# Kernel tuning notes

Hardware: AMD Instinct MI355X
Metric: run time of the kernel (lower is better)

Reference implementation:

```python
import jax, jax.numpy as jnp
import numpy as np

B, S, D, H = 4, 2048, 1024, 16
HD = D // H  # head_dim = 64


def setup_inputs() -> dict:
    key = jax.random.key(0)
    k1, k2, k3, k4, k5 = jax.random.split(key, 5)
    x = jax.random.normal(k1, (B, S, D), dtype=jnp.float32)
    # per-head QKV projection weights (H separate Linear(D, 3*HD) layers, batched)
    Wqkv = jax.random.normal(k2, (H, D, 3 * HD), dtype=jnp.float32) * (D ** -0.5)
    bqkv = jax.random.normal(k3, (H, 3 * HD), dtype=jnp.float32) * 0.02
    # output projection Linear(D, D)
    Wo = jax.random.normal(k4, (D, D), dtype=jnp.float32) * (D ** -0.5)
    bo = jax.random.normal(k5, (D,), dtype=jnp.float32) * 0.02
    return {"x": x, "Wqkv": Wqkv, "bqkv": bqkv, "Wo": Wo, "bo": bo}


def reference(x, Wqkv, bqkv, Wo, bo):
    # Batched per-head QKV projection: [B,S,D] x [H,D,3*HD] -> [B,H,S,3*HD]
    qkv = jnp.einsum('bsd,hde->bhse', x, Wqkv) + bqkv[None, :, None, :]
    q, k, v = jnp.split(qkv, 3, axis=-1)  # each [B,H,S,HD]
    scale = HD ** -0.5
    scores = jnp.einsum('bhqe,bhke->bhqk', q, k) * scale  # [B,H,S,S]
    causal = jnp.tril(jnp.ones((S, S), dtype=bool))
    scores = jnp.where(causal, scores, -jnp.inf)
    attn = jax.nn.softmax(scores, axis=-1)
    # dropout is identity in eval mode
    out = jnp.einsum('bhqk,bhke->bhqe', attn, v)  # [B,H,S,HD]
    out = jnp.transpose(out, (0, 2, 1, 3)).reshape(B, S, D)  # concat heads
    return out @ Wo + bo
```

## Files before the change

kernel.cpp:

```cpp
#include <hip/hip_runtime.h>
#include <hip/hip_bf16.h>

#define B_ 4
#define S_ 2048
#define D_ 1024
#define H_ 16
#define HD_ 64
#define M_TOK 8192
#define QSCALE 0.18033688f

typedef __attribute__((ext_vector_type(4))) float f32x4;
typedef __attribute__((ext_vector_type(4))) int int4_t;
typedef __attribute__((ext_vector_type(8))) short short8;
typedef __attribute__((ext_vector_type(4))) short short4_t;

__device__ inline short f2bf(float f) {
  unsigned u = __builtin_bit_cast(unsigned, f);
  u += 0x7fff + ((u >> 16) & 1);
  return (short)(u >> 16);
}
__device__ inline short f2bf_trunc(float f) {
  return (short)(__builtin_bit_cast(unsigned, f) >> 16);
}
__device__ inline unsigned pack_bf16_trunc(float lo, float hi) {
  return __builtin_amdgcn_perm(__builtin_bit_cast(unsigned, hi),
                               __builtin_bit_cast(unsigned, lo), 0x07060302u);
}

typedef __attribute__((address_space(1))) const unsigned int gas_u32;
typedef __attribute__((address_space(3))) unsigned int las_u32;
__device__ inline void gload_lds16(const void* g, void* l) {
  __builtin_amdgcn_global_load_lds((gas_u32*)g, (las_u32*)l, 16, 0, 0);
}


__global__ __launch_bounds__(256) void conv_x_kernel(
    const float* __restrict__ x, short* __restrict__ xb) {
  size_t base = ((size_t)blockIdx.x * 256 + threadIdx.x) * 8;
  f32x4 v0 = *reinterpret_cast<const f32x4*>(&x[base]);
  f32x4 v1 = *reinterpret_cast<const f32x4*>(&x[base + 4]);
  short8 o;
  o[0]=f2bf(v0[0]); o[1]=f2bf(v0[1]); o[2]=f2bf(v0[2]); o[3]=f2bf(v0[3]);
  o[4]=f2bf(v1[0]); o[5]=f2bf(v1[1]); o[6]=f2bf(v1[2]); o[7]=f2bf(v1[3]);
  *reinterpret_cast<short8*>(&xb[base]) = o;
}

__global__ __launch_bounds__(256) void conv_wqkv_kernel(
    const float* __restrict__ Wqkv, short* __restrict__ wp) {
  const int h = blockIdx.x;
  const int k0 = blockIdx.y * 32;
  const int tid = threadIdx.x;
  __shared__ short T[192 * 40];
#pragma unroll
  for (int i = 0; i < 6; ++i) {
    int iv = tid + i * 256;
    int k = iv / 48;
    int e4 = (iv % 48) * 4;
    f32x4 v = *reinterpret_cast<const f32x4*>(&Wqkv[((size_t)h * D_ + k0 + k) * 192 + e4]);
#pragma unroll
    for (int j = 0; j < 4; ++j) T[(e4 + j) * 40 + k] = f2bf(v[j]);
  }
  __syncthreads();
#pragma unroll
  for (int i = 0; i < 3; ++i) {
    int u = tid + i * 256;
    int e16 = u >> 6;
    int rem = u & 63;
    int e = e16 * 16 + (rem & 15);
    int k8 = (rem >> 4) * 8;
    short8 o = *reinterpret_cast<const short8*>(&T[e * 40 + k8]);
    *reinterpret_cast<short8*>(
        &wp[(size_t)(h * 12 + e16) * 16384 + blockIdx.y * 512 + rem * 8]) = o;
  }
}

__global__ __launch_bounds__(256) void conv_wo_kernel(
    const float* __restrict__ Wo, short* __restrict__ wp) {
  const int k0 = blockIdx.x * 32;
  const int n0 = blockIdx.y * 128;
  const int tid = threadIdx.x;
  __shared__ short T[128 * 40];
#pragma unroll
  for (int i = 0; i < 4; ++i) {
    int iv = tid + i * 256;
    int k = iv >> 5;
    int n4 = (iv & 31) * 4;
    f32x4 v = *reinterpret_cast<const f32x4*>(&Wo[(size_t)(k0 + k) * 1024 + n0 + n4]);
#pragma unroll
    for (int j = 0; j < 4; ++j) T[(n4 + j) * 40 + k] = f2bf(v[j]);
  }
  __syncthreads();
#pragma unroll
  for (int i = 0; i < 2; ++i) {
    int u = tid + i * 256;
    int ntile = u >> 6;
    int rem = u & 63;
    short8 o = *reinterpret_cast<const short8*>(
        &T[(ntile * 16 + (rem & 15)) * 40 + (rem >> 4) * 8]);
    *reinterpret_cast<short8*>(
        &wp[(size_t)((n0 >> 4) + ntile) * 16384 + blockIdx.x * 512 + rem * 8]) = o;
  }
}

template<int EPI>
__global__ __launch_bounds__(256, 3) void gemm4_kernel(
    const short* __restrict__ A, const short* __restrict__ Bp,
    const float* __restrict__ bias,
    short* __restrict__ qb, short* __restrict__ kb, short* __restrict__ vt,
    float* __restrict__ out) {
  constexpr int KD = 1024;
  const int m0 = blockIdx.x * 128;
  const int n0 = blockIdx.y * 128;
  const int tid = threadIdx.x;
  const int lane = tid & 63, wv = tid >> 6;
  const int wr = wv >> 1, wc = wv & 1;
  const int g = lane >> 4, c = lane & 15;

  __shared__ short As[4 * 4096];

  const f32x4 zero4 = {0.f, 0.f, 0.f, 0.f};
  f32x4 acc[4][4];
#pragma unroll
  for (int i = 0; i < 4; ++i)
#pragma unroll
    for (int j = 0; j < 4; ++j) acc[i][j] = zero4;

  const short* bbase = Bp + (size_t)((n0 + wc * 64) >> 4) * 16384 + lane * 8;
  short8 bb0[4], bb1[4];

  auto LOADB = [&](int t, short8* br) {
#pragma unroll
    for (int nt = 0; nt < 4; ++nt)
      br[nt] = *reinterpret_cast<const short8*>(&bbase[(size_t)nt * 16384 + t * 512]);
  };
  auto STAGE = [&](int kt, int buf) {
    const short* asrc = A + (size_t)m0 * KD + kt * 32;
#pragma unroll
    for (int i = 0; i < 2; ++i) {
      int ch = tid + i * 256;
      int row = ch >> 2;
      int slot = (ch & 3) ^ ((row >> 1) & 3);
      gload_lds16(asrc + (size_t)row * KD + slot * 8, &As[buf * 4096 + ch * 8]);
    }
  };
  const int sread = (g ^ ((c >> 1) & 3)) * 8;
  auto COMP = [&](int buf, short8* br) {
    const short* Ab = &As[buf * 4096];
    short8 a[4];
#pragma unroll
    for (int mt = 0; mt < 4; ++mt)
      a[mt] = *reinterpret_cast<const short8*>(&Ab[(wr * 64 + mt * 16 + c) * 32 + sread]);
    __builtin_amdgcn_s_setprio(1);
#pragma unroll
    for (int mt = 0; mt < 4; ++mt)
#pragma unroll
      for (int nt = 0; nt < 4; ++nt)
        acc[mt][nt] = __builtin_amdgcn_mfma_f32_16x16x32_bf16(a[mt], br[nt], acc[mt][nt], 0, 0, 0);
    __builtin_amdgcn_s_setprio(0);
  };

#define BAR1 __builtin_amdgcn_sched_barrier(0); __builtin_amdgcn_s_barrier(); __builtin_amdgcn_sched_barrier(0)
#define VMW(N) asm volatile("s_waitcnt vmcnt(" #N ")" ::: "memory")

  STAGE(0, 0); STAGE(1, 1); LOADB(0, bb0);

#pragma unroll 1
  for (int p = 0; p < 7; ++p) {
    const int tb = p * 4;
    BAR1; STAGE(tb + 2, 2); LOADB(tb + 1, bb1); VMW(6); BAR1; COMP(0, bb0);
    BAR1; STAGE(tb + 3, 3); LOADB(tb + 2, bb0); VMW(6); BAR1; COMP(1, bb1);
    BAR1; STAGE(tb + 4, 0); LOADB(tb + 3, bb1); VMW(6); BAR1; COMP(2, bb0);
    BAR1; STAGE(tb + 5, 1); LOADB(tb + 4, bb0); VMW(6); BAR1; COMP(3, bb1);
  }
  BAR1; STAGE(30, 2); LOADB(29, bb1); VMW(6); BAR1; COMP(0, bb0);
  BAR1; STAGE(31, 3); LOADB(30, bb0); VMW(6); BAR1; COMP(1, bb1);
  BAR1;               LOADB(31, bb1); VMW(4); BAR1; COMP(2, bb0);
  BAR1;                               VMW(0); BAR1; COMP(3, bb1);

#undef BAR1
#undef VMW

  if (EPI == 0) {
#pragma unroll
    for (int nt = 0; nt < 4; ++nt) {
      int n = n0 + wc * 64 + nt * 16 + c;
      float bv = bias[n];
      int h = n / 192, e = n % 192;
      if (e < 128) {
#pragma unroll
        for (int mt = 0; mt < 4; ++mt) {
          int m_base = m0 + wr * 64 + mt * 16 + g * 4;
          int bb2 = m_base >> 11, s0 = m_base & 2047;
          size_t plane = (size_t)(bb2 * H_ + h) * (S_ * HD_);
          if (e < 64) {
            size_t bp = plane + (size_t)(s0 >> 4) * 1024 + (e >> 3) * 128 + (s0 & 15) * 8 + (e & 7);
#pragma unroll
            for (int r = 0; r < 4; ++r)
              qb[bp + r * 8] = f2bf((acc[mt][nt][r] + bv) * QSCALE);
          } else {
            int ek = e - 64;
            size_t bp = plane + (size_t)(s0 >> 4) * 1024 + (ek >> 3) * 128 + (s0 & 15) * 8 + (ek & 7);
#pragma unroll
            for (int r = 0; r < 4; ++r)
              kb[bp + r * 8] = f2bf(acc[mt][nt][r] + bv);
          }
        }
      } else {
        int hd = e - 128;
#pragma unroll
        for (int mtp = 0; mtp < 2; ++mtp) {
          int mt = mtp * 2;
          int m_base = m0 + wr * 64 + mt * 16 + g * 4;
          int bb2 = m_base >> 11, s0 = m_base & 2047;
          size_t plane = (size_t)(bb2 * H_ + h) * (S_ * HD_);
          size_t bp = plane + (size_t)((hd >> 4) * 64 + (s0 >> 5)) * 512 +
                      ((s0 >> 2) & 3) * 128 + (hd & 15) * 8;
          int4_t pk;
#pragma unroll
          for (int r = 0; r < 4; ++r)
            pk[r] = (int)pack_bf16_trunc(acc[mt][nt][r] + bv, acc[mt + 1][nt][r] + bv);
          *reinterpret_cast<int4_t*>(&vt[bp]) = pk;
        }
      }
    }
  } else {
#pragma unroll
    for (int mt = 0; mt < 4; ++mt) {
#pragma unroll
      for (int nt = 0; nt < 4; ++nt) {
        int n = n0 + wc * 64 + nt * 16 + c;
        float bv = bias[n];
        int m_base = m0 + wr * 64 + mt * 16 + g * 4;
#pragma unroll
        for (int r = 0; r < 4; ++r)
          out[(size_t)(m_base + r) * D_ + n] = acc[mt][nt][r] + bv;
      }
    }
  }
}

struct KF32 { short8 f[4]; };

__device__ __forceinline__ void load_kf32(KF32& k, const short* __restrict__ kbh,
                                          int ktb, int lane) {
#pragma unroll
  for (int cc = 0; cc < 2; ++cc)
#pragma unroll
    for (int t = 0; t < 2; ++t)
      k.f[cc * 2 + t] = *reinterpret_cast<const short8*>(
          &kbh[(size_t)(ktb * 2 + t) * 1024 + cc * 512 + lane * 8]);
}

__global__ __launch_bounds__(256, 3) void attn_kernel(
    const short* __restrict__ qb, const short* __restrict__ kb,
    const short* __restrict__ vt, short* __restrict__ av) {
  const int orig = blockIdx.x;
  const int xcd = orig & 7;
  const int local = orig >> 3;
  const int bh = xcd * 8 + (local & 7);
  const int qt = 15 - (local >> 3);
  const int bb = bh >> 4, h = bh & 15;
  const int tid = threadIdx.x;
  const int lane = tid & 63, wv = tid >> 6;
  const int g = lane >> 4, c = lane & 15;
  const int q0 = qt * 128;
  const int r0 = q0 + wv * 32;

  __shared__ short Ps[4][32 * 40];
  short* Pw = Ps[wv];
  unsigned* Pw32 = reinterpret_cast<unsigned*>(Pw);

  const short* qbh = qb + (size_t)bh * S_ * HD_;
  const short* kbh = kb + (size_t)bh * S_ * HD_;
  const short* vth = vt + (size_t)bh * HD_ * S_;

  short8 ones;
#pragma unroll
  for (int j = 0; j < 8; ++j) ones[j] = (short)0x3F80;

  const f32x4 zero4 = {0.f, 0.f, 0.f, 0.f};

  short8 qf[2][2];
#pragma unroll
  for (int mt = 0; mt < 2; ++mt)
#pragma unroll
    for (int cc = 0; cc < 2; ++cc)
      qf[mt][cc] = *reinterpret_cast<const short8*>(
          &qbh[(size_t)(r0 / 16 + mt) * 1024 + cc * 512 + lane * 8]);

  f32x4 acc_o[2][4];
  f32x4 lacc[2];
#pragma unroll
  for (int mt = 0; mt < 2; ++mt) {
    lacc[mt] = zero4;
#pragma unroll
    for (int nt = 0; nt < 4; ++nt) acc_o[mt][nt] = zero4;
  }

  const int diag = 4 * qt + wv;
  const int nk = diag + 1;

  KF32 kA, kB;
  load_kf32(kA, kbh, 0, lane);

  auto body = [&](int ktb, KF32& kc, KF32& kn) {
    const int k0 = ktb * 32;
    short8 vf[4];
#pragma unroll
    for (int nt = 0; nt < 4; ++nt)
      vf[nt] = *reinterpret_cast<const short8*>(
          &vth[(size_t)(nt * 64 + ktb) * 512 + lane * 8]);
    f32x4 sc[2][2];
#pragma unroll
    for (int mt = 0; mt < 2; ++mt)
#pragma unroll
      for (int t = 0; t < 2; ++t) sc[mt][t] = zero4;
#pragma unroll
    for (int cc = 0; cc < 2; ++cc)
#pragma unroll
      for (int mt = 0; mt < 2; ++mt)
#pragma unroll
        for (int t = 0; t < 2; ++t)
          sc[mt][t] = __builtin_amdgcn_mfma_f32_16x16x32_bf16(
              qf[mt][cc], kc.f[cc * 2 + t], sc[mt][t], 0, 0, 0);
    int ktbn = ktb + 1;
    if (ktbn >= S_ / 32) ktbn = 0;
    load_kf32(kn, kbh, ktbn, lane);
    if (ktb == diag) {
#pragma unroll
      for (int mt = 0; mt < 2; ++mt)
#pragma unroll
        for (int t = 0; t < 2; ++t) {
          const int key = k0 + t * 16 + c;
#pragma unroll
          for (int r = 0; r < 4; ++r) {
            const int qi2 = r0 + mt * 16 + g * 4 + r;
            if (key > qi2) sc[mt][t][r] = -INFINITY;
          }
        }
    }
#pragma unroll
    for (int mt = 0; mt < 2; ++mt)
#pragma unroll
      for (int r = 0; r < 4; ++r) {
        float p0 = __builtin_exp2f(sc[mt][0][r]);
        float p1 = __builtin_exp2f(sc[mt][1][r]);
        Pw32[(mt * 16 + g * 4 + r) * 20 + c] = pack_bf16_trunc(p0, p1);
      }
    short8 pa[2];
#pragma unroll
    for (int mt = 0; mt < 2; ++mt)
      pa[mt] = *reinterpret_cast<const short8*>(&Pw[(mt * 16 + c) * 40 + g * 8]);
#pragma unroll
    for (int mt = 0; mt < 2; ++mt)
      lacc[mt] = __builtin_amdgcn_mfma_f32_16x16x32_bf16(pa[mt], ones, lacc[mt], 0, 0, 0);
#pragma unroll
    for (int mt = 0; mt < 2; ++mt)
#pragma unroll
      for (int nt = 0; nt < 4; ++nt)
        acc_o[mt][nt] = __builtin_amdgcn_mfma_f32_16x16x32_bf16(
            pa[mt], vf[nt], acc_o[mt][nt], 0, 0, 0);
  };

  int ktb = 0;
  for (; ktb + 1 < nk; ktb += 2) {
    body(ktb,     kA, kB);
    body(ktb + 1, kB, kA);
  }
  if (ktb < nk) body(ktb, kA, kB);

#pragma unroll
  for (int mt = 0; mt < 2; ++mt) {
    float inv[4];
#pragma unroll
    for (int r = 0; r < 4; ++r) inv[r] = 1.0f / lacc[mt][r];
#pragma unroll
    for (int nt = 0; nt < 4; ++nt)
#pragma unroll
      for (int r = 0; r < 4; ++r) {
        int R = r0 + mt * 16 + g * 4 + r;
        av[(size_t)(bb * S_ + R) * D_ + h * HD_ + nt * 16 + c] =
            f2bf(acc_o[mt][nt][r] * inv[r]);
      }
  }
}

extern "C" void kernel_launch(void* const* d_in, const int* in_sizes, int n_in,
                              void* d_out, int out_size, void* d_ws, size_t ws_size,
                              hipStream_t stream) {
  const float* x    = (const float*)d_in[0];
  const float* Wqkv = (const float*)d_in[1];
  const float* bqkv = (const float*)d_in[2];
  const float* Wo   = (const float*)d_in[3];
  const float* bo   = (const float*)d_in[4];
  float* out = (float*)d_out;

  const size_t NTOK = (size_t)B_ * H_ * S_ * HD_;
  short* xb    = (short*)d_ws;
  short* wqkvt = xb + (size_t)M_TOK * D_;
  short* wot   = wqkvt + (size_t)3072 * 1024;
  short* qb    = wot + (size_t)1024 * 1024;
  short* kb    = qb + NTOK;
  short* vt    = kb + NTOK;
  short* av    = xb;

  conv_x_kernel   <<<4096, 256, 0, stream>>>(x, xb);
  conv_wqkv_kernel<<<dim3(16, 32), 256, 0, stream>>>(Wqkv, wqkvt);
  conv_wo_kernel  <<<dim3(32, 8), 256, 0, stream>>>(Wo, wot);
  gemm4_kernel<0> <<<dim3(64, 24), 256, 0, stream>>>(xb, wqkvt, bqkv, qb, kb, vt, nullptr);
  attn_kernel     <<<1024, 256, 0, stream>>>(qb, kb, vt, av);
  gemm4_kernel<1> <<<dim3(64, 8), 256, 0, stream>>>(av, wot, bo, nullptr, nullptr, nullptr, out);
}
```

Measured before the change: 160.5 us.

## Restructure GEMM mainloop to 64-wide K stages with triple-buffered LDS

Rewrites the bf16 GEMM main loop so each A stage covers 64 K elements (8-chunk XOR swizzle) in a 3-slot LDS ring instead of 32-wide stages in 4 slots. Each barrier pair now covers two K-halves of MFMA work, and B fragments are prefetched two tiles ahead with four register sets. The aim is to halve barrier and waitcnt overhead per unit of compute. In exchange it uses more LDS (48KB vs 32KB) and more registers, which may cut occupancy at 3 blocks per CU.

```diff
diff --git a/kernel.cpp b/kernel.cpp
--- a/kernel.cpp
+++ b/kernel.cpp
@@ -103,7 +103,7 @@
 }
 
 template<int EPI>
-__global__ __launch_bounds__(256, 3) void gemm4_kernel(
+__global__ __launch_bounds__(256, 3) void gemm5_kernel(
     const short* __restrict__ A, const short* __restrict__ Bp,
     const float* __restrict__ bias,
     short* __restrict__ qb, short* __restrict__ kb, short* __restrict__ vt,
@@ -116,7 +116,7 @@
   const int wr = wv >> 1, wc = wv & 1;
   const int g = lane >> 4, c = lane & 15;
 
-  __shared__ short As[4 * 4096];
+  __shared__ short As[3 * 8192];
 
   const f32x4 zero4 = {0.f, 0.f, 0.f, 0.f};
   f32x4 acc[4][4];
@@ -126,30 +126,31 @@
     for (int j = 0; j < 4; ++j) acc[i][j] = zero4;
 
   const short* bbase = Bp + (size_t)((n0 + wc * 64) >> 4) * 16384 + lane * 8;
-  short8 bb0[4], bb1[4];
+  short8 bb0[4], bb1[4], bb2[4], bb3[4];
 
   auto LOADB = [&](int t, short8* br) {
 #pragma unroll
     for (int nt = 0; nt < 4; ++nt)
       br[nt] = *reinterpret_cast<const short8*>(&bbase[(size_t)nt * 16384 + t * 512]);
   };
-  auto STAGE = [&](int kt, int buf) {
-    const short* asrc = A + (size_t)m0 * KD + kt * 32;
-#pragma unroll
-    for (int i = 0; i < 2; ++i) {
+  auto STAGE64 = [&](int kt64, int buf) {
+    const short* asrc = A + (size_t)m0 * KD + kt64 * 64;
+#pragma unroll
+    for (int i = 0; i < 4; ++i) {
       int ch = tid + i * 256;
-      int row = ch >> 2;
-      int slot = (ch & 3) ^ ((row >> 1) & 3);
-      gload_lds16(asrc + (size_t)row * KD + slot * 8, &As[buf * 4096 + ch * 8]);
+      int row = ch >> 3;
+      int sub = ch & 7;
+      int slot = sub ^ (row & 7);
+      gload_lds16(asrc + (size_t)row * KD + slot * 8, &As[buf * 8192 + ch * 8]);
     }
   };
-  const int sread = (g ^ ((c >> 1) & 3)) * 8;
-  auto COMP = [&](int buf, short8* br) {
-    const short* Ab = &As[buf * 4096];
+  auto COMP = [&](int buf, int kh, short8* br) {
+    const short* Ab = &As[buf * 8192];
+    const int chx = ((g + kh * 4) ^ (c & 7)) * 8;
     short8 a[4];
 #pragma unroll
     for (int mt = 0; mt < 4; ++mt)
-      a[mt] = *reinterpret_cast<const short8*>(&Ab[(wr * 64 + mt * 16 + c) * 32 + sread]);
+      a[mt] = *reinterpret_cast<const short8*>(&Ab[(wr * 64 + mt * 16 + c) * 64 + chx]);
     __builtin_amdgcn_s_setprio(1);
 #pragma unroll
     for (int mt = 0; mt < 4; ++mt)
@@ -162,20 +163,29 @@
 #define BAR1 __builtin_amdgcn_sched_barrier(0); __builtin_amdgcn_s_barrier(); __builtin_amdgcn_sched_barrier(0)
 #define VMW(N) asm volatile("s_waitcnt vmcnt(" #N ")" ::: "memory")
 
-  STAGE(0, 0); STAGE(1, 1); LOADB(0, bb0);
-
+  STAGE64(0, 0); STAGE64(1, 1); LOADB(0, bb0); LOADB(1, bb1);
+
+  int e = 0;
 #pragma unroll 1
   for (int p = 0; p < 7; ++p) {
-    const int tb = p * 4;
-    BAR1; STAGE(tb + 2, 2); LOADB(tb + 1, bb1); VMW(6); BAR1; COMP(0, bb0);
-    BAR1; STAGE(tb + 3, 3); LOADB(tb + 2, bb0); VMW(6); BAR1; COMP(1, bb1);
-    BAR1; STAGE(tb + 4, 0); LOADB(tb + 3, bb1); VMW(6); BAR1; COMP(2, bb0);
-    BAR1; STAGE(tb + 5, 1); LOADB(tb + 4, bb0); VMW(6); BAR1; COMP(3, bb1);
-  }
-  BAR1; STAGE(30, 2); LOADB(29, bb1); VMW(6); BAR1; COMP(0, bb0);
-  BAR1; STAGE(31, 3); LOADB(30, bb0); VMW(6); BAR1; COMP(1, bb1);
-  BAR1;               LOADB(31, bb1); VMW(4); BAR1; COMP(2, bb0);
-  BAR1;                               VMW(0); BAR1; COMP(3, bb1);
+    const int o = (e + 1 == 3) ? 0 : e + 1;
+    const int s = (o + 1 == 3) ? 0 : o + 1;
+    BAR1; STAGE64(2 * p + 2, s); LOADB(4 * p + 2, bb2); LOADB(4 * p + 3, bb3);
+    VMW(12); BAR1;
+    COMP(e, 0, bb0); COMP(e, 1, bb1);
+    BAR1; STAGE64(2 * p + 3, e); LOADB(4 * p + 4, bb0); LOADB(4 * p + 5, bb1);
+    VMW(12); BAR1;
+    COMP(o, 0, bb2); COMP(o, 1, bb3);
+    e = s;
+  }
+  {
+    const int o = (e + 1 == 3) ? 0 : e + 1;
+    BAR1; LOADB(30, bb2); LOADB(31, bb3);
+    VMW(8); BAR1;
+    COMP(e, 0, bb0); COMP(e, 1, bb1);
+    VMW(0);
+    COMP(o, 0, bb2); COMP(o, 1, bb3);
+  }
 
 #undef BAR1
 #undef VMW
@@ -185,20 +195,20 @@
     for (int nt = 0; nt < 4; ++nt) {
       int n = n0 + wc * 64 + nt * 16 + c;
       float bv = bias[n];
-      int h = n / 192, e = n % 192;
-      if (e < 128) {
+      int h = n / 192, ee = n % 192;
+      if (ee < 128) {
 #pragma unroll
         for (int mt = 0; mt < 4; ++mt) {
           int m_base = m0 + wr * 64 + mt * 16 + g * 4;
-          int bb2 = m_base >> 11, s0 = m_base & 2047;
-          size_t plane = (size_t)(bb2 * H_ + h) * (S_ * HD_);
-          if (e < 64) {
-            size_t bp = plane + (size_t)(s0 >> 4) * 1024 + (e >> 3) * 128 + (s0 & 15) * 8 + (e & 7);
+          int bb2i = m_base >> 11, s0 = m_base & 2047;
+          size_t plane = (size_t)(bb2i * H_ + h) * (S_ * HD_);
+          if (ee < 64) {
+            size_t bp = plane + (size_t)(s0 >> 4) * 1024 + (ee >> 3) * 128 + (s0 & 15) * 8 + (ee & 7);
 #pragma unroll
             for (int r = 0; r < 4; ++r)
               qb[bp + r * 8] = f2bf((acc[mt][nt][r] + bv) * QSCALE);
           } else {
-            int ek = e - 64;
+            int ek = ee - 64;
             size_t bp = plane + (size_t)(s0 >> 4) * 1024 + (ek >> 3) * 128 + (s0 & 15) * 8 + (ek & 7);
 #pragma unroll
             for (int r = 0; r < 4; ++r)
@@ -206,13 +216,13 @@
           }
         }
       } else {
-        int hd = e - 128;
+        int hd = ee - 128;
 #pragma unroll
         for (int mtp = 0; mtp < 2; ++mtp) {
           int mt = mtp * 2;
           int m_base = m0 + wr * 64 + mt * 16 + g * 4;
-          int bb2 = m_base >> 11, s0 = m_base & 2047;
-          size_t plane = (size_t)(bb2 * H_ + h) * (S_ * HD_);
+          int bb2i = m_base >> 11, s0 = m_base & 2047;
+          size_t plane = (size_t)(bb2i * H_ + h) * (S_ * HD_);
           size_t bp = plane + (size_t)((hd >> 4) * 64 + (s0 >> 5)) * 512 +
                       ((s0 >> 2) & 3) * 128 + (hd & 15) * 8;
           int4_t pk;
@@ -407,7 +417,7 @@
   conv_x_kernel   <<<4096, 256, 0, stream>>>(x, xb);
   conv_wqkv_kernel<<<dim3(16, 32), 256, 0, stream>>>(Wqkv, wqkvt);
   conv_wo_kernel  <<<dim3(32, 8), 256, 0, stream>>>(Wo, wot);
-  gemm4_kernel<0> <<<dim3(64, 24), 256, 0, stream>>>(xb, wqkvt, bqkv, qb, kb, vt, nullptr);
+  gemm5_kernel<0> <<<dim3(64, 24), 256, 0, stream>>>(xb, wqkvt, bqkv, qb, kb, vt, nullptr);
   attn_kernel     <<<1024, 256, 0, stream>>>(qb, kb, vt, av);
-  gemm4_kernel<1> <<<dim3(64, 8), 256, 0, stream>>>(av, wot, bo, nullptr, nullptr, nullptr, out);
-}
+  gemm5_kernel<1> <<<dim3(64, 8), 256, 0, stream>>>(av, wot, bo, nullptr, nullptr, nullptr, out);
+}
```

After: 177.5 us. +10.6%, slower.

## Replace QKV projection GEMM with 256x128-tile 512-thread kernel and XCD-aware mapping

Applied to the files above, without the earlier changes.

The QKV projection GEMM moves to a new kernel using 512-thread blocks with 256x128 output tiles and K-steps of 64 held in swizzled LDS. A triple-buffered register set for B fragments is fully unrolled, and a 1D grid remaps block ids so each XCD handles a fixed group of N columns. The aim is more reuse per loaded A tile, fewer barriers per K step, and better L2 locality across XCDs. In exchange it uses 128KB LDS and one block per CU, which lowers occupancy. The output projection keeps the old kernel, now specialized without the template epilogue switch.

```diff
diff --git a/kernel.cpp b/kernel.cpp
--- a/kernel.cpp
+++ b/kernel.cpp
@@ -102,12 +102,148 @@
   }
 }
 
-template<int EPI>
-__global__ __launch_bounds__(256, 3) void gemm4_kernel(
+__global__ __launch_bounds__(512, 1) void gemm8_kernel(
     const short* __restrict__ A, const short* __restrict__ Bp,
     const float* __restrict__ bias,
-    short* __restrict__ qb, short* __restrict__ kb, short* __restrict__ vt,
-    float* __restrict__ out) {
+    short* __restrict__ qb, short* __restrict__ kb, short* __restrict__ vt) {
+  constexpr int KD = 1024;
+  const int bid = blockIdx.x;
+  const int xcd = bid & 7;
+  const int local = bid >> 3;
+  const int m0 = (local / 3) * 256;
+  const int n0 = (xcd * 3 + local % 3) * 128;
+  const int tid = threadIdx.x;
+  const int lane = tid & 63, wv = tid >> 6;
+  const int wm = wv >> 1, wn = wv & 1;
+  const int g = lane >> 4, c = lane & 15;
+
+  __shared__ short As[4 * 16384];
+
+  const f32x4 zero4 = {0.f, 0.f, 0.f, 0.f};
+  f32x4 acc[4][4];
+#pragma unroll
+  for (int i = 0; i < 4; ++i)
+#pragma unroll
+    for (int j = 0; j < 4; ++j) acc[i][j] = zero4;
+
+  const short* bbase = Bp + (size_t)((n0 + wn * 64) >> 4) * 16384 + lane * 8;
+  short8 sA[8], sB[8], sC[8];
+
+  auto STAGE64 = [&](int kt64, int buf) {
+    const short* asrc = A + (size_t)m0 * KD + kt64 * 64;
+#pragma unroll
+    for (int i = 0; i < 4; ++i) {
+      int ch = tid + i * 512;
+      int row = ch >> 3;
+      int slot = (ch & 7) ^ (row & 7);
+      gload_lds16(asrc + (size_t)row * KD + slot * 8, &As[buf * 16384 + ch * 8]);
+    }
+  };
+
+#define LOADBH(TAU, SET, KH) { \
+  _Pragma("unroll") \
+  for (int nt = 0; nt < 4; ++nt) \
+    SET[(KH) * 4 + nt] = *reinterpret_cast<const short8*>( \
+        &bbase[(size_t)nt * 16384 + (TAU) * 512]); }
+
+#define COMPH(BUF, KH, SET) { \
+  const short* Ab = &As[(BUF) * 16384]; \
+  const int chx = ((g + (KH) * 4) ^ (c & 7)) * 8; \
+  short8 a[4]; \
+  _Pragma("unroll") \
+  for (int mt = 0; mt < 4; ++mt) \
+    a[mt] = *reinterpret_cast<const short8*>(&Ab[(wm * 64 + mt * 16 + c) * 64 + chx]); \
+  __builtin_amdgcn_s_setprio(1); \
+  _Pragma("unroll") \
+  for (int mt = 0; mt < 4; ++mt) \
+    _Pragma("unroll") \
+    for (int nt = 0; nt < 4; ++nt) \
+      acc[mt][nt] = __builtin_amdgcn_mfma_f32_16x16x32_bf16(a[mt], SET[(KH) * 4 + nt], acc[mt][nt], 0, 0, 0); \
+  __builtin_amdgcn_s_setprio(0); }
+
+#define BAR1 __builtin_amdgcn_sched_barrier(0); __builtin_amdgcn_s_barrier(); __builtin_amdgcn_sched_barrier(0)
+#define VMW(N) asm volatile("s_waitcnt vmcnt(" #N ")" ::: "memory")
+
+#define TILE(T, LB, SB, BC, BN) \
+  BAR1; STAGE64((T) + 2, SB); LOADBH(2 * ((T) + 2), BN, 0); VMW(20); BAR1; \
+  COMPH(LB, 0, BC); \
+  LOADBH(2 * ((T) + 2) + 1, BN, 1); \
+  COMPH(LB, 1, BC);
+
+  STAGE64(0, 0); STAGE64(1, 1);
+  LOADBH(0, sA, 0); LOADBH(1, sA, 1);
+  LOADBH(2, sB, 0); LOADBH(3, sB, 1);
+
+  TILE(0,  0, 2, sA, sC)
+  TILE(1,  1, 3, sB, sA)
+  TILE(2,  2, 0, sC, sB)
+  TILE(3,  3, 1, sA, sC)
+  TILE(4,  0, 2, sB, sA)
+  TILE(5,  1, 3, sC, sB)
+  TILE(6,  2, 0, sA, sC)
+  TILE(7,  3, 1, sB, sA)
+  TILE(8,  0, 2, sC, sB)
+  TILE(9,  1, 3, sA, sC)
+  TILE(10, 2, 0, sB, sA)
+  TILE(11, 3, 1, sC, sB)
+  TILE(12, 0, 2, sA, sC)
+  TILE(13, 1, 3, sB, sA)
+  BAR1; VMW(12); BAR1; COMPH(2, 0, sC); COMPH(2, 1, sC);
+  BAR1; VMW(0);  BAR1; COMPH(3, 0, sA); COMPH(3, 1, sA);
+
+#undef TILE
+#undef BAR1
+#undef VMW
+#undef LOADBH
+#undef COMPH
+
+#pragma unroll
+  for (int nt = 0; nt < 4; ++nt) {
+    int n = n0 + wn * 64 + nt * 16 + c;
+    float bv = bias[n];
+    int h = n / 192, e = n % 192;
+    if (e < 128) {
+#pragma unroll
+      for (int mt = 0; mt < 4; ++mt) {
+        int m_base = m0 + wm * 64 + mt * 16 + g * 4;
+        int bb2 = m_base >> 11, s0 = m_base & 2047;
+        size_t plane = (size_t)(bb2 * H_ + h) * (S_ * HD_);
+        if (e < 64) {
+          size_t bp = plane + (size_t)(s0 >> 4) * 1024 + (e >> 3) * 128 + (s0 & 15) * 8 + (e & 7);
+#pragma unroll
+          for (int r = 0; r < 4; ++r)
+            qb[bp + r * 8] = f2bf((acc[mt][nt][r] + bv) * QSCALE);
+        } else {
+          int ek = e - 64;
+          size_t bp = plane + (size_t)(s0 >> 4) * 1024 + (ek >> 3) * 128 + (s0 & 15) * 8 + (ek & 7);
+#pragma unroll
+          for (int r = 0; r < 4; ++r)
+            kb[bp + r * 8] = f2bf(acc[mt][nt][r] + bv);
+        }
+      }
+    } else {
+      int hd = e - 128;
+#pragma unroll
+      for (int mtp = 0; mtp < 2; ++mtp) {
+        int mt = mtp * 2;
+        int m_base = m0 + wm * 64 + mt * 16 + g * 4;
+        int bb2 = m_base >> 11, s0 = m_base & 2047;
+        size_t plane = (size_t)(bb2 * H_ + h) * (S_ * HD_);
+        size_t bp = plane + (size_t)((hd >> 4) * 64 + (s0 >> 5)) * 512 +
+                    ((s0 >> 2) & 3) * 128 + (hd & 15) * 8;
+        int4_t pk;
+#pragma unroll
+        for (int r = 0; r < 4; ++r)
+          pk[r] = (int)pack_bf16_trunc(acc[mt][nt][r] + bv, acc[mt + 1][nt][r] + bv);
+        *reinterpret_cast<int4_t*>(&vt[bp]) = pk;
+      }
+    }
+  }
+}
+
+__global__ __launch_bounds__(256, 3) void gemm4p_kernel(
+    const short* __restrict__ A, const short* __restrict__ Bp,
+    const float* __restrict__ bias, float* __restrict__ out) {
   constexpr int KD = 1024;
   const int m0 = blockIdx.x * 128;
   const int n0 = blockIdx.y * 128;
@@ -180,61 +316,16 @@
 #undef BAR1
 #undef VMW
 
-  if (EPI == 0) {
+#pragma unroll
+  for (int mt = 0; mt < 4; ++mt) {
 #pragma unroll
     for (int nt = 0; nt < 4; ++nt) {
       int n = n0 + wc * 64 + nt * 16 + c;
       float bv = bias[n];
-      int h = n / 192, e = n % 192;
-      if (e < 128) {
-#pragma unroll
-        for (int mt = 0; mt < 4; ++mt) {
-          int m_base = m0 + wr * 64 + mt * 16 + g * 4;
-          int bb2 = m_base >> 11, s0 = m_base & 2047;
-          size_t plane = (size_t)(bb2 * H_ + h) * (S_ * HD_);
-          if (e < 64) {
-            size_t bp = plane + (size_t)(s0 >> 4) * 1024 + (e >> 3) * 128 + (s0 & 15) * 8 + (e & 7);
-#pragma unroll
-            for (int r = 0; r < 4; ++r)
-              qb[bp + r * 8] = f2bf((acc[mt][nt][r] + bv) * QSCALE);
-          } else {
-            int ek = e - 64;
-            size_t bp = plane + (size_t)(s0 >> 4) * 1024 + (ek >> 3) * 128 + (s0 & 15) * 8 + (ek & 7);
-#pragma unroll
-            for (int r = 0; r < 4; ++r)
-              kb[bp + r * 8] = f2bf(acc[mt][nt][r] + bv);
-          }
-        }
-      } else {
-        int hd = e - 128;
-#pragma unroll
-        for (int mtp = 0; mtp < 2; ++mtp) {
-          int mt = mtp * 2;
-          int m_base = m0 + wr * 64 + mt * 16 + g * 4;
-          int bb2 = m_base >> 11, s0 = m_base & 2047;
-          size_t plane = (size_t)(bb2 * H_ + h) * (S_ * HD_);
-          size_t bp = plane + (size_t)((hd >> 4) * 64 + (s0 >> 5)) * 512 +
-                      ((s0 >> 2) & 3) * 128 + (hd & 15) * 8;
-          int4_t pk;
-#pragma unroll
-          for (int r = 0; r < 4; ++r)
-            pk[r] = (int)pack_bf16_trunc(acc[mt][nt][r] + bv, acc[mt + 1][nt][r] + bv);
-          *reinterpret_cast<int4_t*>(&vt[bp]) = pk;
-        }
-      }
-    }
-  } else {
-#pragma unroll
-    for (int mt = 0; mt < 4; ++mt) {
-#pragma unroll
-      for (int nt = 0; nt < 4; ++nt) {
-        int n = n0 + wc * 64 + nt * 16 + c;
-        float bv = bias[n];
-        int m_base = m0 + wr * 64 + mt * 16 + g * 4;
-#pragma unroll
-        for (int r = 0; r < 4; ++r)
-          out[(size_t)(m_base + r) * D_ + n] = acc[mt][nt][r] + bv;
-      }
+      int m_base = m0 + wr * 64 + mt * 16 + g * 4;
+#pragma unroll
+      for (int r = 0; r < 4; ++r)
+        out[(size_t)(m_base + r) * D_ + n] = acc[mt][nt][r] + bv;
     }
   }
 }
@@ -407,7 +498,7 @@
   conv_x_kernel   <<<4096, 256, 0, stream>>>(x, xb);
   conv_wqkv_kernel<<<dim3(16, 32), 256, 0, stream>>>(Wqkv, wqkvt);
   conv_wo_kernel  <<<dim3(32, 8), 256, 0, stream>>>(Wo, wot);
-  gemm4_kernel<0> <<<dim3(64, 24), 256, 0, stream>>>(xb, wqkvt, bqkv, qb, kb, vt, nullptr);
+  gemm8_kernel    <<<768, 512, 0, stream>>>(xb, wqkvt, bqkv, qb, kb, vt);
   attn_kernel     <<<1024, 256, 0, stream>>>(qb, kb, vt, av);
-  gemm4_kernel<1> <<<dim3(64, 8), 256, 0, stream>>>(av, wot, bo, nullptr, nullptr, nullptr, out);
-}
+  gemm4p_kernel   <<<dim3(64, 8), 256, 0, stream>>>(av, wot, bo, out);
+}
```

Result: slower. 168.3 us (+4.9%).
